# Optimization experiments

Measured on AMD Instinct MI355X. Metric: run time of the kernel, lower is better.

Reference implementation:

```python
import jax, jax.numpy as jnp
import numpy as np

WH, WW = 12, 12          # window size
NUM_HEADS = 12
DIM = 384
CPB_HIDDEN = 512


def _relative_coords_table():
    # (1, 2*Wh-1, 2*Ww-1, 2), log-scaled continuous relative coords (pretrained_window_size == 0 path)
    ch = np.arange(-(WH - 1), WH, dtype=np.float32)
    cw = np.arange(-(WW - 1), WW, dtype=np.float32)
    t = np.stack(np.meshgrid(ch, cw, indexing='ij'), axis=-1)[None]  # (1, 2Wh-1, 2Ww-1, 2)
    t = t.copy()
    t[..., 0] /= (WH - 1)
    t[..., 1] /= (WW - 1)
    t = t * 8.0
    t = np.sign(t) * np.log2(np.abs(t) + 1.0) / np.log2(8.0)
    return jnp.asarray(t, dtype=jnp.float32)


def _relative_position_index():
    ch = np.arange(WH)
    cw = np.arange(WW)
    coords = np.stack(np.meshgrid(ch, cw, indexing='ij'))          # (2, Wh, Ww)
    cf = coords.reshape(2, -1)                                      # (2, N)
    rel = (cf[:, :, None] - cf[:, None, :]).transpose(1, 2, 0)      # (N, N, 2)
    rel[..., 0] += WH - 1
    rel[..., 1] += WW - 1
    rel[..., 0] *= 2 * WW - 1
    return jnp.asarray(rel.sum(-1), dtype=jnp.int32)                # (N, N)


def _l2_normalize(x):
    rnorm = jax.lax.rsqrt(jnp.maximum(jnp.sum(x * x, axis=-1, keepdims=True), 1e-12))
    return x * rnorm


def setup_inputs() -> dict:
    key = jax.random.key(0)
    ks = jax.random.split(key, 10)
    B_, N, C = 512, WH * WW, DIM
    s = lambda fan_in: 1.0 / np.sqrt(fan_in)
    return {
        'x': jax.random.normal(ks[0], (B_, N, C), dtype=jnp.float32),
        'w_qkv': jax.random.normal(ks[1], (C, 3 * C), dtype=jnp.float32) * s(C),
        'q_bias': jnp.zeros((C,), dtype=jnp.float32),
        'v_bias': jnp.zeros((C,), dtype=jnp.float32),
        'logit_scale': jnp.log(10.0 * jnp.ones((NUM_HEADS, 1, 1), dtype=jnp.float32)),
        'cpb_w1': jax.random.normal(ks[2], (2, CPB_HIDDEN), dtype=jnp.float32) * s(2),
        'cpb_b1': jnp.zeros((CPB_HIDDEN,), dtype=jnp.float32),
        'cpb_w2': jax.random.normal(ks[3], (CPB_HIDDEN, NUM_HEADS), dtype=jnp.float32) * s(CPB_HIDDEN),
        'proj_w': jax.random.normal(ks[4], (C, C), dtype=jnp.float32) * s(C),
        'proj_b': jnp.zeros((C,), dtype=jnp.float32),
    }


def reference(x, w_qkv, q_bias, v_bias, logit_scale, cpb_w1, cpb_b1, cpb_w2, proj_w, proj_b):
    B_, N, C = x.shape
    H = NUM_HEADS
    Dh = C // H

    # qkv projection (no bias in Dense) + manual qkv bias with zero k-bias
    qkv_bias = jnp.concatenate([q_bias, jnp.zeros_like(v_bias), v_bias])
    qkv = x @ w_qkv + qkv_bias                                  # (B_, N, 3C)
    qkv = qkv.reshape(B_, N, 3, H, Dh).transpose(2, 0, 3, 1, 4)  # (3, B_, H, N, Dh)
    q, k, v = qkv[0], qkv[1], qkv[2]

    # cosine attention with learnable clamped temperature
    qn = _l2_normalize(q)
    kn = _l2_normalize(k)
    scale = jnp.exp(jnp.minimum(logit_scale, np.log(100.0)))     # (H, 1, 1)
    attn = jnp.einsum('bhnd,bhmd->bhnm', qn, kn) * scale         # (B_, H, N, N)

    # continuous position bias (CPB) MLP over the relative coords table
    table = _relative_coords_table()                             # (1, 2Wh-1, 2Ww-1, 2)
    bias_table = jnp.maximum(table @ cpb_w1 + cpb_b1, 0.0) @ cpb_w2   # (1, 2Wh-1, 2Ww-1, H)
    bias_table = bias_table.reshape(-1, H)                       # ((2Wh-1)*(2Ww-1), H)
    rpi = _relative_position_index().reshape(-1)                 # (N*N,)
    rel_bias = bias_table[rpi].reshape(N, N, H).transpose(2, 0, 1)  # (H, N, N)
    rel_bias = 16.0 * jax.nn.sigmoid(rel_bias)
    attn = attn + rel_bias[None]                                 # broadcast over B_

    attn = jax.nn.softmax(attn, axis=-1)
    out = jnp.einsum('bhnm,bhmd->bhnd', attn, v)                 # (B_, H, N, Dh)
    out = out.transpose(0, 2, 1, 3).reshape(B_, N, C)
    return out @ proj_w + proj_b
```

## Files before the change

kernel.cpp:

```cpp
#include <hip/hip_runtime.h>
#include <hip/hip_bf16.h>
#include <cstdint>
#include <cstddef>

typedef __attribute__((ext_vector_type(8))) short short8;
typedef __attribute__((ext_vector_type(4))) float f32x4;

__device__ __forceinline__ float b2f(ushort u) {
  union { float f; uint32_t i; } x; x.i = ((uint32_t)u) << 16; return x.f;
}
__device__ __forceinline__ ushort f2b(float f) {
  uint32_t i = __builtin_bit_cast(uint32_t, f);
  i += 0x7fffu + ((i >> 16) & 1u);
  return (ushort)(i >> 16);
}
__device__ __forceinline__ f32x4 mfma16(short8 a, short8 b, f32x4 c) {
  asm("v_mfma_f32_16x16x32_bf16 %0, %1, %2, %0" : "+v"(c) : "v"(a), "v"(b));
  return c;
}
__device__ __forceinline__ void gload_lds16(const void* g, void* l) {
  auto gp = reinterpret_cast<const __attribute__((address_space(1))) uint32_t*>(
      reinterpret_cast<uintptr_t>(g));
  auto lp = reinterpret_cast<__attribute__((address_space(3))) uint32_t*>(
      reinterpret_cast<uintptr_t>(l));
  __builtin_amdgcn_global_load_lds(gp, lp, 16, 0, 0);
}

__global__ __launch_bounds__(256) void k_cvtx(const float* __restrict__ x, ushort* __restrict__ o) {
  size_t i = (size_t)blockIdx.x * 256 + threadIdx.x;
  const float4* xp = (const float4*)x;
  float4 a = xp[i * 2], b = xp[i * 2 + 1];
  union { short8 v; ushort u[8]; } r;
  r.u[0] = f2b(a.x); r.u[1] = f2b(a.y); r.u[2] = f2b(a.z); r.u[3] = f2b(a.w);
  r.u[4] = f2b(b.x); r.u[5] = f2b(b.y); r.u[6] = f2b(b.z); r.u[7] = f2b(b.w);
  *(short8*)&o[i * 8] = r.v;
}

__global__ __launch_bounds__(256) void k_cvtT(const float* __restrict__ W, ushort* __restrict__ Wt,
                                              int R, int C) {
  int r = blockIdx.x;
  for (int c = threadIdx.x; c < C; c += 256)
    Wt[(size_t)c * R + r] = f2b(W[(size_t)r * C + c]);
}

__device__ __forceinline__ float cpb_coord(int i) {
  float v = (float)(i - 11) * (8.0f / 11.0f);
  float l = log2f(fabsf(v) + 1.0f) * (1.0f / 3.0f);
  return v < 0.0f ? -l : l;
}

__global__ void k_cpb1(const float* __restrict__ w1, const float* __restrict__ b1,
                       const float* __restrict__ w2, float* __restrict__ bt) {
  int e = blockIdx.x;
  float t0 = cpb_coord(e / 23);
  float t1 = cpb_coord(e % 23);
  float acc[12];
#pragma unroll
  for (int h = 0; h < 12; h++) acc[h] = 0.0f;
  for (int u = threadIdx.x; u < 512; u += 64) {
    float hv = fmaxf(fmaf(t0, w1[u], fmaf(t1, w1[512 + u], b1[u])), 0.0f);
#pragma unroll
    for (int h = 0; h < 12; h++) acc[h] = fmaf(hv, w2[u * 12 + h], acc[h]);
  }
#pragma unroll
  for (int h = 0; h < 12; h++)
    for (int m = 1; m < 64; m <<= 1) acc[h] += __shfl_xor(acc[h], m);
  if (threadIdx.x == 0) {
#pragma unroll
    for (int h = 0; h < 12; h++) bt[e * 12 + h] = acc[h];
  }
}

__global__ void k_cpb2(const float* __restrict__ bt, float* __restrict__ rb) {
  int h = blockIdx.x / 144, i = blockIdx.x % 144;
  int j = threadIdx.x;
  if (j >= 144) return;
  int yi = i / 12, xi = i % 12, yj = j / 12, xj = j % 12;
  int idx = (yi - yj + 11) * 23 + (xi - xj + 11);
  float v = bt[idx * 12 + h];
  rb[((size_t)h * 144 + i) * 144 + j] = 16.0f / (1.0f + expf(-v));
}

template <int EPI>
__global__ __launch_bounds__(256) void k_gemm(
    const ushort* __restrict__ A, const ushort* __restrict__ Bt, int K, int NB,
    const float* __restrict__ bias0, const float* __restrict__ bias1,
    ushort* __restrict__ O0, ushort* __restrict__ O1, ushort* __restrict__ O2,
    float* __restrict__ FO) {
  __shared__ __align__(16) ushort Smem[2 * 128 * 64];
  ushort* As = Smem;
  ushort* Bs = Smem + 128 * 64;
  const int tid = threadIdx.x;
  const int lane = tid & 63, w = tid >> 6;
  const int wr = w >> 1, wc = w & 1;
  const int l15 = lane & 15, g = lane >> 4;

  const int per = gridDim.x >> 3;
  const int bid = (blockIdx.x & 7) * per + (blockIdx.x >> 3);
  const int bm = bid / NB, bn = bid % NB;

  f32x4 acc[4][4];
#pragma unroll
  for (int m = 0; m < 4; m++)
#pragma unroll
    for (int n = 0; n < 4; n++) acc[m][n] = (f32x4){0.f, 0.f, 0.f, 0.f};

  const size_t arow0 = (size_t)bm * 128;
  const size_t brow0 = (size_t)bn * 128;

  const int srow = lane >> 3;
  const int sblk0 = (lane & 7) ^ srow;
  const size_t soff = (size_t)srow * K + sblk0 * 8;

  for (int k0 = 0; k0 < K; k0 += 64) {
#pragma unroll
    for (int i = 0; i < 4; i++) {
      int c = i * 4 + w;
      gload_lds16(&A[(arow0 + c * 8) * (size_t)K + k0 + soff], &As[c * 512]);
      gload_lds16(&Bt[(brow0 + c * 8) * (size_t)K + k0 + soff], &Bs[c * 512]);
    }
    __syncthreads();
#pragma unroll
    for (int ks = 0; ks < 2; ks++) {
      short8 af[4], bf[4];
#pragma unroll
      for (int m = 0; m < 4; m++) {
        int row = wr * 64 + m * 16 + l15;
        af[m] = *(const short8*)&As[row * 64 + (((ks * 4 + g) ^ (row & 7)) << 3)];
      }
#pragma unroll
      for (int n = 0; n < 4; n++) {
        int row = wc * 64 + n * 16 + l15;
        bf[n] = *(const short8*)&Bs[row * 64 + (((ks * 4 + g) ^ (row & 7)) << 3)];
      }
#pragma unroll
      for (int m = 0; m < 4; m++)
#pragma unroll
        for (int n = 0; n < 4; n++) acc[m][n] = mfma16(af[m], bf[n], acc[m][n]);
    }
    __syncthreads();
  }

  unsigned char* Cb = (unsigned char*)Smem;

  if (EPI == 0) {
    const int sec = bn / 3;
    const int cbase = (bn - sec * 3) * 128;
    if (sec == 2) {
      float vb4[4];
#pragma unroll
      for (int n = 0; n < 4; n++) vb4[n] = bias1[cbase + wc * 64 + n * 16 + l15];
#pragma unroll
      for (int m = 0; m < 4; m++) {
        int rbase = bm * 128 + wr * 64 + m * 16 + g * 4;
        int b = rbase / 144, nn = rbase - b * 144;
#pragma unroll
        for (int n = 0; n < 4; n++) {
          int cc = cbase + wc * 64 + n * 16 + l15;
          int head = cc >> 5, d = cc & 31;
          ushort4 pk;
          pk.x = f2b(acc[m][n][0] + vb4[n]);
          pk.y = f2b(acc[m][n][1] + vb4[n]);
          pk.z = f2b(acc[m][n][2] + vb4[n]);
          pk.w = f2b(acc[m][n][3] + vb4[n]);
          *(ushort4*)&O2[(((size_t)b * 12 + head) * 32 + d) * 144 + nn] = pk;
        }
      }
    } else {
      float bn4[4];
#pragma unroll
      for (int n = 0; n < 4; n++)
        bn4[n] = (sec == 0) ? bias0[cbase + wc * 64 + n * 16 + l15] : 0.0f;
#pragma unroll
      for (int m = 0; m < 4; m++)
#pragma unroll
        for (int n = 0; n < 4; n++) {
          int col = wc * 64 + n * 16 + l15;
#pragma unroll
          for (int e = 0; e < 4; e++) {
            int row = wr * 64 + m * 16 + g * 4 + e;
            int sblk = (col >> 3) ^ ((row >> 2) & 7);
            *(ushort*)&Cb[row * 256 + sblk * 16 + (col & 7) * 2] =
                f2b(acc[m][n][e] + bn4[n]);
          }
        }
      __syncthreads();
      int r = tid >> 1, half = tid & 1;
      int grow = bm * 128 + r;
      int b = grow / 144, nn = grow - b * 144;
      ushort* dst = (sec == 0) ? O0 : O1;
#pragma unroll
      for (int j = 0; j < 8; j++) {
        int lb = half * 8 + j;
        int sblk = lb ^ ((r >> 2) & 7);
        uint4 v = *(uint4*)&Cb[r * 256 + sblk * 16];
        int c0 = cbase + lb * 8;
        int head = c0 >> 5, d0 = c0 & 31;
        *(uint4*)&dst[(((size_t)b * 12 + head) * 144 + nn) * 32 + d0] = v;
      }
    }
  } else {
    float bn4[4];
#pragma unroll
    for (int n = 0; n < 4; n++) bn4[n] = bias0[bn * 128 + wc * 64 + n * 16 + l15];
#pragma unroll
    for (int p = 0; p < 2; p++) {
      if (wc == p) {
#pragma unroll
        for (int m = 0; m < 4; m++)
#pragma unroll
          for (int n = 0; n < 4; n++) {
            int lcol = n * 16 + l15;
#pragma unroll
            for (int e = 0; e < 4; e++) {
              int row = wr * 64 + m * 16 + g * 4 + e;
              int sblk = (lcol >> 2) ^ ((row >> 2) & 7);
              *(float*)&Cb[row * 256 + sblk * 16 + (lcol & 3) * 4] =
                  acc[m][n][e] + bn4[n];
            }
          }
      }
      __syncthreads();
      int r = tid >> 1, half = tid & 1;
#pragma unroll
      for (int j = 0; j < 8; j++) {
        int lb = half * 8 + j;
        int sblk = lb ^ ((r >> 2) & 7);
        uint4 v = *(uint4*)&Cb[r * 256 + sblk * 16];
        *(uint4*)&FO[(size_t)(bm * 128 + r) * 384 + bn * 128 + p * 64 + lb * 4] = v;
      }
      __syncthreads();
    }
  }
}

__global__ __launch_bounds__(256) void k_attn(
    const ushort* __restrict__ Qg, const ushort* __restrict__ Kg, const ushort* __restrict__ VTg,
    const float* __restrict__ lsc, const float* __restrict__ relb, ushort* __restrict__ AO) {
  __shared__ ushort Qs[144 * 40];
  __shared__ ushort Ks[144 * 40];
  __shared__ ushort Vt[32 * 168];
  __shared__ ushort Pw[4][16 * 168];
  __shared__ float rq[144], rk[144];

  const int tid = threadIdx.x;
  const int lane = tid & 63, w = tid >> 6;
  const int l15 = lane & 15, g = lane >> 4;
  const int bh = blockIdx.x;
  const int b = bh / 12, h = bh % 12;
  const size_t base = (size_t)bh * 4608;

  for (int f = tid; f < 576; f += 256) {
    int row = f >> 2, oct = f & 3;
    *(uint4*)&Qs[row * 40 + oct * 8] = *(const uint4*)&Qg[base + row * 32 + oct * 8];
    *(uint4*)&Ks[row * 40 + oct * 8] = *(const uint4*)&Kg[base + row * 32 + oct * 8];
  }
  for (int f = tid; f < 576; f += 256) {
    int d = f / 18, j = f % 18;
    *(uint4*)&Vt[d * 168 + j * 8] = *(const uint4*)&VTg[base + d * 144 + j * 8];
  }
  if (tid < 64) {
    int d = tid >> 1, j = tid & 1;
    *(uint4*)&Vt[d * 168 + 144 + j * 8] = (uint4){0, 0, 0, 0};
  }
  if (lane < 32) {
    int r = lane >> 1, j = lane & 1;
    *(uint4*)&Pw[w][r * 168 + 144 + j * 8] = (uint4){0, 0, 0, 0};
  }
  __syncthreads();

  for (int r = tid; r < 288; r += 256) {
    int rr = r < 144 ? r : r - 144;
    const ushort* src = (r < 144 ? Qs : Ks) + rr * 40;
    float s = 0.f;
#pragma unroll
    for (int d = 0; d < 32; d++) { float xv = b2f(src[d]); s = fmaf(xv, xv, s); }
    float rv = rsqrtf(fmaxf(s, 1e-12f));
    if (r < 144) rq[rr] = rv; else rk[rr] = rv;
  }
  __syncthreads();

  const float sc = __expf(fminf(lsc[h], 4.6051702f));
  const float* rbh = relb + (size_t)h * (144 * 144);

  for (int ti = w; ti < 9; ti += 4) {
    short8 aq = *(const short8*)&Qs[(ti * 16 + l15) * 40 + g * 8];
    f32x4 s[9];
#pragma unroll
    for (int tj = 0; tj < 9; tj++) {
      short8 bk = *(const short8*)&Ks[(tj * 16 + l15) * 40 + g * 8];
      f32x4 z = {0.f, 0.f, 0.f, 0.f};
      s[tj] = mfma16(aq, bk, z);
    }
    const int rloc = g * 4;
    float rqv[4];
#pragma unroll
    for (int e = 0; e < 4; e++) rqv[e] = rq[ti * 16 + rloc + e] * sc;

    float lg[9][4];
#pragma unroll
    for (int tj = 0; tj < 9; tj++) {
      float rkv = rk[tj * 16 + l15];
      const float* rbp = rbh + (size_t)(ti * 16 + rloc) * 144 + tj * 16 + l15;
#pragma unroll
      for (int e = 0; e < 4; e++)
        lg[tj][e] = fmaf(s[tj][e] * rqv[e], rkv, rbp[(size_t)e * 144]);
    }

    float inv[4];
#pragma unroll
    for (int e = 0; e < 4; e++) {
      float m = lg[0][e];
#pragma unroll
      for (int tj = 1; tj < 9; tj++) m = fmaxf(m, lg[tj][e]);
      m = fmaxf(m, __shfl_xor(m, 1));
      m = fmaxf(m, __shfl_xor(m, 2));
      m = fmaxf(m, __shfl_xor(m, 4));
      m = fmaxf(m, __shfl_xor(m, 8));
      float ssum = 0.f;
#pragma unroll
      for (int tj = 0; tj < 9; tj++) { lg[tj][e] = __expf(lg[tj][e] - m); ssum += lg[tj][e]; }
      ssum += __shfl_xor(ssum, 1);
      ssum += __shfl_xor(ssum, 2);
      ssum += __shfl_xor(ssum, 4);
      ssum += __shfl_xor(ssum, 8);
      inv[e] = 1.0f / ssum;
    }

#pragma unroll
    for (int tj = 0; tj < 9; tj++)
#pragma unroll
      for (int e = 0; e < 4; e++)
        Pw[w][(rloc + e) * 168 + tj * 16 + l15] = f2b(lg[tj][e] * inv[e]);

    asm volatile("s_waitcnt lgkmcnt(0)" ::: "memory");
    __builtin_amdgcn_sched_barrier(0);

#pragma unroll
    for (int dt = 0; dt < 2; dt++) {
      f32x4 o = {0.f, 0.f, 0.f, 0.f};
#pragma unroll
      for (int ks = 0; ks < 5; ks++) {
        short8 ap = *(const short8*)&Pw[w][l15 * 168 + ks * 32 + g * 8];
        short8 bv = *(const short8*)&Vt[(dt * 16 + l15) * 168 + ks * 32 + g * 8];
        o = mfma16(ap, bv, o);
      }
      ushort* dst = &AO[((size_t)b * 144 + ti * 16 + rloc) * 384 + h * 32 + dt * 16 + l15];
#pragma unroll
      for (int e = 0; e < 4; e++) dst[(size_t)e * 384] = f2b(o[e]);
    }
  }
}

extern "C" void kernel_launch(void* const* d_in, const int* in_sizes, int n_in,
                              void* d_out, int out_size, void* d_ws, size_t ws_size,
                              hipStream_t stream) {
  const float* x     = (const float*)d_in[0];
  const float* wqkv  = (const float*)d_in[1];
  const float* qbias = (const float*)d_in[2];
  const float* vbias = (const float*)d_in[3];
  const float* lsc   = (const float*)d_in[4];
  const float* cw1   = (const float*)d_in[5];
  const float* cb1   = (const float*)d_in[6];
  const float* cw2   = (const float*)d_in[7];
  const float* pw    = (const float*)d_in[8];
  const float* pb    = (const float*)d_in[9];

  char* ws = (char*)d_ws;
  ushort* xb = (ushort*)(ws);
  ushort* wt = (ushort*)(ws + 56623104);
  ushort* pt = (ushort*)(ws + 57507840);
  ushort* qb = (ushort*)(ws + 57802752);
  ushort* kb = (ushort*)(ws + 114425856);
  ushort* vb = (ushort*)(ws + 171048960);
  float*  bt = (float*)(ws + 227672064);
  float*  rb = (float*)(ws + 227697456);
  ushort* ao = xb;

  k_cvtx<<<13824, 256, 0, stream>>>(x, xb);
  k_cvtT<<<384, 256, 0, stream>>>(wqkv, wt, 384, 1152);
  k_cvtT<<<384, 256, 0, stream>>>(pw, pt, 384, 384);
  k_cpb1<<<529, 64, 0, stream>>>(cw1, cb1, cw2, bt);
  k_cpb2<<<1728, 144, 0, stream>>>(bt, rb);
  k_gemm<0><<<5184, 256, 0, stream>>>(xb, wt, 384, 9, qbias, vbias, qb, kb, vb, nullptr);
  k_attn<<<6144, 256, 0, stream>>>(qb, kb, vb, lsc, rb, ao);
  k_gemm<1><<<1728, 256, 0, stream>>>(ao, pt, 384, 3, pb, nullptr, nullptr, nullptr, nullptr, (float*)d_out);
}
```

Before: 335.7 us.

## Fuse Q/K norm into load, swizzle LDS, hoist K fragments, raise occupancy

Result: faster. 304.5 us (-9.3%).

```diff
diff --git a/kernel.cpp b/kernel.cpp
--- a/kernel.cpp
+++ b/kernel.cpp
@@ -234,11 +234,11 @@
   }
 }
 
-__global__ __launch_bounds__(256) void k_attn(
+__global__ __launch_bounds__(256, 3) void k_attn(
     const ushort* __restrict__ Qg, const ushort* __restrict__ Kg, const ushort* __restrict__ VTg,
     const float* __restrict__ lsc, const float* __restrict__ relb, ushort* __restrict__ AO) {
-  __shared__ ushort Qs[144 * 40];
-  __shared__ ushort Ks[144 * 40];
+  __shared__ ushort Qs[144 * 32];
+  __shared__ ushort Ks[144 * 32];
   __shared__ ushort Vt[32 * 168];
   __shared__ ushort Pw[4][16 * 168];
   __shared__ float rq[144], rk[144];
@@ -252,8 +252,24 @@
 
   for (int f = tid; f < 576; f += 256) {
     int row = f >> 2, oct = f & 3;
-    *(uint4*)&Qs[row * 40 + oct * 8] = *(const uint4*)&Qg[base + row * 32 + oct * 8];
-    *(uint4*)&Ks[row * 40 + oct * 8] = *(const uint4*)&Kg[base + row * 32 + oct * 8];
+    union { uint4 v; ushort u[8]; } qv, kv;
+    qv.v = *(const uint4*)&Qg[base + row * 32 + oct * 8];
+    kv.v = *(const uint4*)&Kg[base + row * 32 + oct * 8];
+    int blk = (oct ^ (row & 3)) << 3;
+    *(uint4*)&Qs[row * 32 + blk] = qv.v;
+    *(uint4*)&Ks[row * 32 + blk] = kv.v;
+    float sq = 0.f, sk = 0.f;
+#pragma unroll
+    for (int j = 0; j < 8; j++) {
+      float xq = b2f(qv.u[j]); sq = fmaf(xq, xq, sq);
+      float xk = b2f(kv.u[j]); sk = fmaf(xk, xk, sk);
+    }
+    sq += __shfl_xor(sq, 1); sq += __shfl_xor(sq, 2);
+    sk += __shfl_xor(sk, 1); sk += __shfl_xor(sk, 2);
+    if (oct == 0) {
+      rq[row] = rsqrtf(fmaxf(sq, 1e-12f));
+      rk[row] = rsqrtf(fmaxf(sk, 1e-12f));
+    }
   }
   for (int f = tid; f < 576; f += 256) {
     int d = f / 18, j = f % 18;
@@ -269,28 +285,26 @@
   }
   __syncthreads();
 
-  for (int r = tid; r < 288; r += 256) {
-    int rr = r < 144 ? r : r - 144;
-    const ushort* src = (r < 144 ? Qs : Ks) + rr * 40;
-    float s = 0.f;
-#pragma unroll
-    for (int d = 0; d < 32; d++) { float xv = b2f(src[d]); s = fmaf(xv, xv, s); }
-    float rv = rsqrtf(fmaxf(s, 1e-12f));
-    if (r < 144) rq[rr] = rv; else rk[rr] = rv;
-  }
-  __syncthreads();
+  short8 kf[9];
+  float rkv9[9];
+#pragma unroll
+  for (int tj = 0; tj < 9; tj++) {
+    int R = tj * 16 + l15;
+    kf[tj] = *(const short8*)&Ks[R * 32 + ((g ^ (R & 3)) << 3)];
+    rkv9[tj] = rk[R];
+  }
 
   const float sc = __expf(fminf(lsc[h], 4.6051702f));
   const float* rbh = relb + (size_t)h * (144 * 144);
 
   for (int ti = w; ti < 9; ti += 4) {
-    short8 aq = *(const short8*)&Qs[(ti * 16 + l15) * 40 + g * 8];
+    int RQ = ti * 16 + l15;
+    short8 aq = *(const short8*)&Qs[RQ * 32 + ((g ^ (RQ & 3)) << 3)];
     f32x4 s[9];
 #pragma unroll
     for (int tj = 0; tj < 9; tj++) {
-      short8 bk = *(const short8*)&Ks[(tj * 16 + l15) * 40 + g * 8];
       f32x4 z = {0.f, 0.f, 0.f, 0.f};
-      s[tj] = mfma16(aq, bk, z);
+      s[tj] = mfma16(aq, kf[tj], z);
     }
     const int rloc = g * 4;
     float rqv[4];
@@ -300,11 +314,10 @@
     float lg[9][4];
 #pragma unroll
     for (int tj = 0; tj < 9; tj++) {
-      float rkv = rk[tj * 16 + l15];
       const float* rbp = rbh + (size_t)(ti * 16 + rloc) * 144 + tj * 16 + l15;
 #pragma unroll
       for (int e = 0; e < 4; e++)
-        lg[tj][e] = fmaf(s[tj][e] * rqv[e], rkv, rbp[(size_t)e * 144]);
+        lg[tj][e] = fmaf(s[tj][e] * rqv[e], rkv9[tj], rbp[(size_t)e * 144]);
     }
 
     float inv[4];
```
